# Kernel tuning notes

Hardware: AMD Instinct MI355X
Metric: run time of the kernel (lower is better)

## Reference

```python
import jax, jax.numpy as jnp
import numpy as np

B, N, D, O = 128, 256, 512, 512
EPS = 1e-5


def setup_inputs() -> dict:
    key = jax.random.key(0)
    ks = jax.random.split(key, 12)
    Observation = jax.random.normal(ks[0], (B, N, D), dtype=jnp.float32)
    mask = jax.random.bernoulli(ks[1], 0.7, (B, N))
    s = 0.02
    W1 = jax.random.normal(ks[2], (D, O), dtype=jnp.float32) * s
    W2 = jax.random.normal(ks[3], (O, O), dtype=jnp.float32) * s
    W3 = jax.random.normal(ks[4], (O, O), dtype=jnp.float32) * s
    g1 = 1.0 + 0.1 * jax.random.normal(ks[5], (D,), dtype=jnp.float32)
    b1 = 0.02 * jax.random.normal(ks[6], (D,), dtype=jnp.float32)
    g2 = 1.0 + 0.1 * jax.random.normal(ks[7], (O,), dtype=jnp.float32)
    b2 = 0.02 * jax.random.normal(ks[8], (O,), dtype=jnp.float32)
    g3 = 1.0 + 0.1 * jax.random.normal(ks[9], (O,), dtype=jnp.float32)
    b3 = 0.02 * jax.random.normal(ks[10], (O,), dtype=jnp.float32)
    return {"Observation": Observation, "mask": mask,
            "g1": g1, "b1": b1, "W1": W1,
            "g2": g2, "b2": b2, "W2": W2,
            "g3": g3, "b3": b3, "W3": W3}


def layer_norm(x, g, b):
    m = jnp.mean(x, axis=-1, keepdims=True)
    v = jnp.mean(jnp.square(x - m), axis=-1, keepdims=True)
    return (x - m) * jax.lax.rsqrt(v + EPS) * g + b


def reference(Observation, mask, g1, b1, W1, g2, b2, W2, g3, b3, W3):
    Bv, Nv, Dv = Observation.shape
    # _grant_at_least_one_valid: force element 0 valid if a row is all-invalid
    all_invalid = ~jnp.any(mask, axis=1)  # [B]
    mask = mask | (all_invalid[:, None] & (jnp.arange(Nv) == 0)[None, :])
    x = Observation.reshape(-1, Dv)  # [B*N, D]
    # Block 1: LN -> Linear (no bias) -> Tanh (dropout is eval identity)
    h1 = jnp.tanh(layer_norm(x, g1, b1) @ W1)
    # Block 2
    h2 = jnp.tanh(layer_norm(h1, g2, b2) @ W2)
    # Block 3 with residual input (h2 + h1), no activation
    o3 = layer_norm(h2 + h1, g3, b3) @ W3  # [B*N, O]
    fill = jnp.finfo(o3.dtype).min
    o3 = jnp.where(mask.reshape(-1, 1), o3, fill)
    out = jax.nn.softmax(o3.reshape(Bv, Nv, -1), axis=1)
    return jnp.nan_to_num(out, nan=0.0)
```

## Files before the change

kernel.cpp:

```cpp
#include <hip/hip_runtime.h>


#define NN 256

typedef _Float16 f16;
typedef __attribute__((ext_vector_type(4))) _Float16 f16x4;
typedef __attribute__((ext_vector_type(8))) _Float16 f16x8;
typedef __attribute__((ext_vector_type(4))) float f32x4;

#define XS    520
#define EPS32 516

__device__ __forceinline__ float fast_tanh(float x) {
  float e = __expf(2.f * x);
  return 1.f - 2.f * __builtin_amdgcn_rcpf(e + 1.f);
}
__device__ __forceinline__ void async_copy16(const void* g, void* l) {
  __builtin_amdgcn_global_load_lds(
      (const __attribute__((address_space(1))) unsigned int*)g,
      (__attribute__((address_space(3))) unsigned int*)l, 16, 0, 0);
}

__global__ void prep_w_kernel(const float* __restrict__ W1, const float* __restrict__ W2,
                              const float* __restrict__ W3, f16* __restrict__ WT) {
  int idx = blockIdx.x * 256 + threadIdx.x;
  int s   = idx >> 18;
  int rem = idx & 0x3FFFF;
  int o   = rem >> 9;
  int d   = rem & 511;
  const float* W = (s == 0) ? W1 : (s == 1) ? W2 : W3;
  WT[idx] = (f16)W[d * 512 + o];
}

__device__ __forceinline__ void stage_b(const f16* __restrict__ Bg, f16* __restrict__ dst,
                                        int wv, int lane, int c) {
  #pragma unroll
  for (int q = 0; q < 4; ++q) {
    int r0 = wv * 64 + q * 16;
    const f16* gb = Bg + (((size_t)(r0 + (lane >> 2))) << 9) + c * 32 + (lane & 3) * 8;
    async_copy16(gb, dst + r0 * 32);
  }
}

__global__ __launch_bounds__(512, 2) void mega_kernel(
    const float* __restrict__ Obs,
    const float* __restrict__ g1, const float* __restrict__ b1,
    const f16* __restrict__ WT,
    const float* __restrict__ g2, const float* __restrict__ b2,
    const float* __restrict__ g3, const float* __restrict__ b3,
    float* __restrict__ outF) {
  __shared__ __align__(16) char smem[136704];
  f16* sX  = (f16*)smem;
  f16* sB0 = (f16*)(smem + 66560);
  f16* sB1 = (f16*)(smem + 99328);
  float2* sPart = (float2*)(smem + 132096);
  float2* sStat = (float2*)(smem + 136192);

  int t = threadIdx.x, lane = t & 63, wv = t >> 6;
  int row16 = lane & 15, quad = lane >> 4;
  int rBase = blockIdx.x * 64;

  stage_b(WT, sB0, wv, lane, 0);

  {
    float4 w0 = *(const float4*)(g1 + lane * 4);
    float4 u0 = *(const float4*)(b1 + lane * 4);
    float4 w1 = *(const float4*)(g1 + 256 + lane * 4);
    float4 u1 = *(const float4*)(b1 + 256 + lane * 4);
    #pragma unroll
    for (int p = 0; p < 8; ++p) {
      int row = wv * 8 + p;
      const float* x = Obs + (((size_t)(rBase + row)) << 9);
      float4 v0 = *(const float4*)(x + lane * 4);
      float4 v1 = *(const float4*)(x + 256 + lane * 4);
      float s = v0.x + v0.y + v0.z + v0.w + v1.x + v1.y + v1.z + v1.w;
      float q = v0.x*v0.x + v0.y*v0.y + v0.z*v0.z + v0.w*v0.w
              + v1.x*v1.x + v1.y*v1.y + v1.z*v1.z + v1.w*v1.w;
      #pragma unroll
      for (int off = 1; off < 64; off <<= 1) {
        s += __shfl_xor(s, off, 64);
        q += __shfl_xor(q, off, 64);
      }
      float mean = s * (1.f / 512.f);
      float var  = q * (1.f / 512.f) - mean * mean;
      float inv  = 1.f / sqrtf(var + 1e-5f);
      f16x4 o0, o1;
      o0[0] = (f16)((v0.x - mean) * inv * w0.x + u0.x);
      o0[1] = (f16)((v0.y - mean) * inv * w0.y + u0.y);
      o0[2] = (f16)((v0.z - mean) * inv * w0.z + u0.z);
      o0[3] = (f16)((v0.w - mean) * inv * w0.w + u0.w);
      o1[0] = (f16)((v1.x - mean) * inv * w1.x + u1.x);
      o1[1] = (f16)((v1.y - mean) * inv * w1.y + u1.y);
      o1[2] = (f16)((v1.z - mean) * inv * w1.z + u1.z);
      o1[3] = (f16)((v1.w - mean) * inv * w1.w + u1.w);
      *(f16x4*)&sX[row * XS + lane * 4] = o0;
      *(f16x4*)&sX[row * XS + 256 + lane * 4] = o1;
    }
  }

  f32x4 acc[4][4];
  f16x4 h1s[4][4];

  __syncthreads();

  for (int g = 0; g < 3; ++g) {
    const f16* Bg = WT + ((size_t)g << 18);

    #pragma unroll
    for (int mi = 0; mi < 4; ++mi)
      #pragma unroll
      for (int ni = 0; ni < 4; ++ni)
        acc[mi][ni] = (f32x4){0.f, 0.f, 0.f, 0.f};

    for (int c = 0; c < 16; ++c) {
      if (c < 15) stage_b(Bg, (c & 1) ? sB0 : sB1, wv, lane, c + 1);

      const f16* bb = (c & 1) ? sB1 : sB0;
      f16x8 af[4], bf[4];
      #pragma unroll
      for (int i = 0; i < 4; ++i) {
        int ar = i * 16 + row16;
        af[i] = *(const f16x8*)&sX[ar * XS + c * 32 + quad * 8];
        int br = wv * 64 + i * 16 + row16;
        bf[i] = *(const f16x8*)&bb[br * 32 + quad * 8];
      }
      #pragma unroll
      for (int mi = 0; mi < 4; ++mi)
        #pragma unroll
        for (int ni = 0; ni < 4; ++ni)
          acc[mi][ni] = __builtin_amdgcn_mfma_f32_16x16x32_f16(af[mi], bf[ni], acc[mi][ni], 0, 0, 0);

      __syncthreads();
    }

    if (g == 2) {
      float* sE = (float*)smem;
      #pragma unroll
      for (int half = 0; half < 2; ++half) {
        #pragma unroll
        for (int mi = 0; mi < 2; ++mi) {
          int rt = half * 2 + mi;
          #pragma unroll
          for (int ni = 0; ni < 4; ++ni) {
            int col = wv * 64 + ni * 16 + row16;
            #pragma unroll
            for (int rg = 0; rg < 4; ++rg)
              sE[(mi * 16 + quad * 4 + rg) * EPS32 + col] = acc[rt][ni][rg];
          }
        }
        __syncthreads();
        #pragma unroll
        for (int i = 0; i < 8; ++i) {
          int gi = t + i * 512;
          int row = gi >> 7, cg = (gi & 127) * 4;
          f32x4 v = *(const f32x4*)&sE[row * EPS32 + cg];
          *(f32x4*)&outF[(((size_t)(rBase + half * 32 + row)) << 9) + cg] = v;
        }
        __syncthreads();
      }
    } else {
      #pragma unroll
      for (int mi = 0; mi < 4; ++mi)
        #pragma unroll
        for (int ni = 0; ni < 4; ++ni)
          #pragma unroll
          for (int rg = 0; rg < 4; ++rg)
            acc[mi][ni][rg] = fast_tanh(acc[mi][ni][rg]);

      if (g == 0) {
        #pragma unroll
        for (int mi = 0; mi < 4; ++mi)
          #pragma unroll
          for (int ni = 0; ni < 4; ++ni) {
            f16x4 h;
            #pragma unroll
            for (int rg = 0; rg < 4; ++rg) h[rg] = (f16)acc[mi][ni][rg];
            h1s[mi][ni] = h;
          }
      } else {
        #pragma unroll
        for (int mi = 0; mi < 4; ++mi)
          #pragma unroll
          for (int ni = 0; ni < 4; ++ni)
            #pragma unroll
            for (int rg = 0; rg < 4; ++rg)
              acc[mi][ni][rg] += (float)h1s[mi][ni][rg];
      }

      stage_b(WT + ((size_t)(g + 1) << 18), sB0, wv, lane, 0);

      const float* gp = (g == 0) ? g2 : g3;
      const float* bp = (g == 0) ? b2 : b3;
      float gva[4], bva[4];
      #pragma unroll
      for (int ni = 0; ni < 4; ++ni) {
        int col = wv * 64 + ni * 16 + row16;
        gva[ni] = gp[col]; bva[ni] = bp[col];
      }

      #pragma unroll
      for (int mi = 0; mi < 4; ++mi)
        #pragma unroll
        for (int rg = 0; rg < 4; ++rg) {
          float s = 0.f, q = 0.f;
          #pragma unroll
          for (int ni = 0; ni < 4; ++ni) {
            float v = acc[mi][ni][rg];
            s += v; q += v * v;
          }
          #pragma unroll
          for (int off = 1; off < 16; off <<= 1) {
            s += __shfl_xor(s, off, 16);
            q += __shfl_xor(q, off, 16);
          }
          if (row16 == 0)
            sPart[wv * 64 + mi * 16 + quad * 4 + rg] = make_float2(s, q);
        }
      __syncthreads();
      if (t < 64) {
        float s = 0.f, q = 0.f;
        #pragma unroll
        for (int w = 0; w < 8; ++w) {
          float2 p = sPart[w * 64 + t];
          s += p.x; q += p.y;
        }
        float mean = s * (1.f / 512.f);
        float var  = q * (1.f / 512.f) - mean * mean;
        sStat[t] = make_float2(mean, 1.f / sqrtf(var + 1e-5f));
      }
      __syncthreads();

      #pragma unroll
      for (int mi = 0; mi < 4; ++mi)
        #pragma unroll
        for (int rg = 0; rg < 4; ++rg) {
          int row = mi * 16 + quad * 4 + rg;
          float2 st = sStat[row];
          #pragma unroll
          for (int ni = 0; ni < 4; ++ni) {
            int col = wv * 64 + ni * 16 + row16;
            sX[row * XS + col] = (f16)((acc[mi][ni][rg] - st.x) * st.y * gva[ni] + bva[ni]);
          }
        }
      __syncthreads();
    }
  }
}

__global__ __launch_bounds__(256, 2) void softmax_kernel(const float* __restrict__ o3,
                                                         const int* __restrict__ mask,
                                                         float* __restrict__ out) {
  __shared__ float sz[NN * 64];
  __shared__ float sredm[4 * 64];
  __shared__ float sreds[4 * 64];
  __shared__ int   smask[NN];

  int b  = blockIdx.x >> 3;
  int oc = blockIdx.x & 7;
  int t  = threadIdx.x;
  int o_l = t & 63;
  int n_h = t >> 6;

  int mt = mask[b * NN + t];
  int any = __syncthreads_or(mt);
  smask[t] = (t == 0 && !any) ? 1 : mt;
  __syncthreads();

  const float* src = o3 + (((size_t)(b * NN)) << 9) + oc * 64;
  #pragma unroll 4
  for (int j = 0; j < 64; ++j) {
    int n = j * 4 + n_h;
    float v = src[((size_t)n << 9) + o_l];
    sz[n * 64 + o_l] = smask[n] ? v : -3.4e38f;
  }
  __syncthreads();

  float mx = -3.4e38f;
  #pragma unroll 8
  for (int i = 0; i < 64; ++i)
    mx = fmaxf(mx, sz[(n_h * 64 + i) * 64 + o_l]);
  sredm[n_h * 64 + o_l] = mx;
  __syncthreads();
  float m4 = fmaxf(fmaxf(sredm[o_l], sredm[64 + o_l]),
                   fmaxf(sredm[128 + o_l], sredm[192 + o_l]));

  float sm = 0.f;
  #pragma unroll 8
  for (int i = 0; i < 64; ++i)
    sm += __expf(sz[(n_h * 64 + i) * 64 + o_l] - m4);
  sreds[n_h * 64 + o_l] = sm;
  __syncthreads();
  float tot = sreds[o_l] + sreds[64 + o_l] + sreds[128 + o_l] + sreds[192 + o_l];
  float inv = 1.f / tot;

  float* dst = out + (((size_t)(b * NN)) << 9) + oc * 64;
  #pragma unroll 4
  for (int j = 0; j < 64; ++j) {
    int n = j * 4 + n_h;
    dst[((size_t)n << 9) + o_l] = __expf(sz[n * 64 + o_l] - m4) * inv;
  }
}

extern "C" void kernel_launch(void* const* d_in, const int* in_sizes, int n_in,
                              void* d_out, int out_size, void* d_ws, size_t ws_size,
                              hipStream_t stream) {
  const float* Obs = (const float*)d_in[0];
  const int*   msk = (const int*)d_in[1];
  const float* g1  = (const float*)d_in[2];
  const float* b1  = (const float*)d_in[3];
  const float* W1  = (const float*)d_in[4];
  const float* g2  = (const float*)d_in[5];
  const float* b2  = (const float*)d_in[6];
  const float* W2  = (const float*)d_in[7];
  const float* g3  = (const float*)d_in[8];
  const float* b3  = (const float*)d_in[9];
  const float* W3  = (const float*)d_in[10];
  float* out = (float*)d_out;

  char* ws = (char*)d_ws;
  const size_t MB = 1u << 20;
  float* Lg = (float*)ws;
  f16*   WT = (f16*)(ws + 64 * MB);

  prep_w_kernel<<<3072, 256, 0, stream>>>(W1, W2, W3, WT);
  mega_kernel<<<512, 512, 0, stream>>>(Obs, g1, b1, WT, g2, b2, g3, b3, Lg);
  softmax_kernel<<<1024, 256, 0, stream>>>(Lg, msk, out);
}
```

Before: 325.4 us.

## Load weight fragments directly into registers and keep softmax columns in registers

The GEMM loop no longer stages weight tiles through LDS with async copies. Each wave now loads its B fragments straight from global memory (L2) into registers, double-buffering them across k-steps. This removes the per-step barriers and shrinks LDS from about 137KB to 71KB, which may allow more blocks per CU, but makes the MFMA loop depend on global-load latency. The softmax kernel is also rewritten to hold each thread's 16 float4 values in registers with vectorized loads and stores, replacing the large LDS staging buffer.

```diff
diff --git a/kernel.cpp b/kernel.cpp
--- a/kernel.cpp
+++ b/kernel.cpp
@@ -14,11 +14,6 @@
 __device__ __forceinline__ float fast_tanh(float x) {
   float e = __expf(2.f * x);
   return 1.f - 2.f * __builtin_amdgcn_rcpf(e + 1.f);
-}
-__device__ __forceinline__ void async_copy16(const void* g, void* l) {
-  __builtin_amdgcn_global_load_lds(
-      (const __attribute__((address_space(1))) unsigned int*)g,
-      (__attribute__((address_space(3))) unsigned int*)l, 16, 0, 0);
 }
 
 __global__ void prep_w_kernel(const float* __restrict__ W1, const float* __restrict__ W2,
@@ -32,14 +27,17 @@
   WT[idx] = (f16)W[d * 512 + o];
 }
 
-__device__ __forceinline__ void stage_b(const f16* __restrict__ Bg, f16* __restrict__ dst,
-                                        int wv, int lane, int c) {
-  #pragma unroll
-  for (int q = 0; q < 4; ++q) {
-    int r0 = wv * 64 + q * 16;
-    const f16* gb = Bg + (((size_t)(r0 + (lane >> 2))) << 9) + c * 32 + (lane & 3) * 8;
-    async_copy16(gb, dst + r0 * 32);
-  }
+__device__ __forceinline__ void gemm_step(f32x4 acc[4][4], const f16* __restrict__ sXb,
+                                          const f16x8 bf[4], int c) {
+  f16x8 af[4];
+  #pragma unroll
+  for (int i = 0; i < 4; ++i)
+    af[i] = *(const f16x8*)&sXb[i * 16 * XS + c * 32];
+  #pragma unroll
+  for (int mi = 0; mi < 4; ++mi)
+    #pragma unroll
+    for (int ni = 0; ni < 4; ++ni)
+      acc[mi][ni] = __builtin_amdgcn_mfma_f32_16x16x32_f16(af[mi], bf[ni], acc[mi][ni], 0, 0, 0);
 }
 
 __global__ __launch_bounds__(512, 2) void mega_kernel(
@@ -49,18 +47,24 @@
     const float* __restrict__ g2, const float* __restrict__ b2,
     const float* __restrict__ g3, const float* __restrict__ b3,
     float* __restrict__ outF) {
-  __shared__ __align__(16) char smem[136704];
-  f16* sX  = (f16*)smem;
-  f16* sB0 = (f16*)(smem + 66560);
-  f16* sB1 = (f16*)(smem + 99328);
-  float2* sPart = (float2*)(smem + 132096);
-  float2* sStat = (float2*)(smem + 136192);
+  __shared__ __align__(16) char smem[71168];
+  f16* sX = (f16*)smem;
+  float2* sPart = (float2*)(smem + 66560);
+  float2* sStat = (float2*)(smem + 70656);
 
   int t = threadIdx.x, lane = t & 63, wv = t >> 6;
   int row16 = lane & 15, quad = lane >> 4;
   int rBase = blockIdx.x * 64;
 
-  stage_b(WT, sB0, wv, lane, 0);
+  const f16* sXb = sX + row16 * XS + quad * 8;
+  const f16* bw  = WT + (((size_t)(wv * 64 + row16)) << 9) + quad * 8;
+
+  f32x4 acc[4][4];
+  f16x8 bfA[4], bfB[4];
+  f16x4 h1s[4][4];
+
+  #pragma unroll
+  for (int i = 0; i < 4; ++i) bfA[i] = *(const f16x8*)(bw + i * 8192);
 
   {
     float4 w0 = *(const float4*)(g1 + lane * 4);
@@ -97,43 +101,31 @@
       *(f16x4*)&sX[row * XS + 256 + lane * 4] = o1;
     }
   }
-
-  f32x4 acc[4][4];
-  f16x4 h1s[4][4];
-
   __syncthreads();
 
   for (int g = 0; g < 3; ++g) {
-    const f16* Bg = WT + ((size_t)g << 18);
-
     #pragma unroll
     for (int mi = 0; mi < 4; ++mi)
       #pragma unroll
       for (int ni = 0; ni < 4; ++ni)
         acc[mi][ni] = (f32x4){0.f, 0.f, 0.f, 0.f};
 
-    for (int c = 0; c < 16; ++c) {
-      if (c < 15) stage_b(Bg, (c & 1) ? sB0 : sB1, wv, lane, c + 1);
-
-      const f16* bb = (c & 1) ? sB1 : sB0;
-      f16x8 af[4], bf[4];
-      #pragma unroll
-      for (int i = 0; i < 4; ++i) {
-        int ar = i * 16 + row16;
-        af[i] = *(const f16x8*)&sX[ar * XS + c * 32 + quad * 8];
-        int br = wv * 64 + i * 16 + row16;
-        bf[i] = *(const f16x8*)&bb[br * 32 + quad * 8];
-      }
-      #pragma unroll
-      for (int mi = 0; mi < 4; ++mi)
-        #pragma unroll
-        for (int ni = 0; ni < 4; ++ni)
-          acc[mi][ni] = __builtin_amdgcn_mfma_f32_16x16x32_f16(af[mi], bf[ni], acc[mi][ni], 0, 0, 0);
-
+    #pragma unroll
+    for (int c = 0; c < 16; c += 2) {
+      #pragma unroll
+      for (int i = 0; i < 4; ++i)
+        bfB[i] = *(const f16x8*)(bw + i * 8192 + (c + 1) * 32);
+      gemm_step(acc, sXb, bfA, c);
+      if (c + 2 < 16) {
+        #pragma unroll
+        for (int i = 0; i < 4; ++i)
+          bfA[i] = *(const f16x8*)(bw + i * 8192 + (c + 2) * 32);
+      }
+      gemm_step(acc, sXb, bfB, c + 1);
+    }
+
+    if (g == 2) {
       __syncthreads();
-    }
-
-    if (g == 2) {
       float* sE = (float*)smem;
       #pragma unroll
       for (int half = 0; half < 2; ++half) {
@@ -187,8 +179,6 @@
               acc[mi][ni][rg] += (float)h1s[mi][ni][rg];
       }
 
-      stage_b(WT + ((size_t)(g + 1) << 18), sB0, wv, lane, 0);
-
       const float* gp = (g == 0) ? g2 : g3;
       const float* bp = (g == 0) ? b2 : b3;
       float gva[4], bva[4];
@@ -228,6 +218,11 @@
         float var  = q * (1.f / 512.f) - mean * mean;
         sStat[t] = make_float2(mean, 1.f / sqrtf(var + 1e-5f));
       }
+
+      bw += 262144;
+      #pragma unroll
+      for (int i = 0; i < 4; ++i) bfA[i] = *(const f16x8*)(bw + i * 8192);
+
       __syncthreads();
 
       #pragma unroll
@@ -250,54 +245,73 @@
 __global__ __launch_bounds__(256, 2) void softmax_kernel(const float* __restrict__ o3,
                                                          const int* __restrict__ mask,
                                                          float* __restrict__ out) {
-  __shared__ float sz[NN * 64];
-  __shared__ float sredm[4 * 64];
-  __shared__ float sreds[4 * 64];
-  __shared__ int   smask[NN];
+  __shared__ float4 smx[16][16];
+  __shared__ float4 sms[16][16];
+  __shared__ int    smask[NN];
 
   int b  = blockIdx.x >> 3;
   int oc = blockIdx.x & 7;
   int t  = threadIdx.x;
-  int o_l = t & 63;
-  int n_h = t >> 6;
+  int c4 = t & 15;
+  int nh = t >> 4;
+
+  const float4* src = (const float4*)(o3 + (((size_t)(b * NN)) << 9)) + oc * 16 + c4;
+  float4 v[16];
+  #pragma unroll
+  for (int j = 0; j < 16; ++j)
+    v[j] = src[(size_t)(nh + 16 * j) * 128];
 
   int mt = mask[b * NN + t];
   int any = __syncthreads_or(mt);
   smask[t] = (t == 0 && !any) ? 1 : mt;
   __syncthreads();
 
-  const float* src = o3 + (((size_t)(b * NN)) << 9) + oc * 64;
-  #pragma unroll 4
-  for (int j = 0; j < 64; ++j) {
-    int n = j * 4 + n_h;
-    float v = src[((size_t)n << 9) + o_l];
-    sz[n * 64 + o_l] = smask[n] ? v : -3.4e38f;
-  }
+  const float NEG = -3.4e38f;
+  #pragma unroll
+  for (int j = 0; j < 16; ++j)
+    if (!smask[nh + 16 * j]) v[j] = (float4){NEG, NEG, NEG, NEG};
+
+  float4 m4 = v[0];
+  #pragma unroll
+  for (int j = 1; j < 16; ++j) {
+    m4.x = fmaxf(m4.x, v[j].x); m4.y = fmaxf(m4.y, v[j].y);
+    m4.z = fmaxf(m4.z, v[j].z); m4.w = fmaxf(m4.w, v[j].w);
+  }
+  smx[nh][c4] = m4;
   __syncthreads();
-
-  float mx = -3.4e38f;
-  #pragma unroll 8
-  for (int i = 0; i < 64; ++i)
-    mx = fmaxf(mx, sz[(n_h * 64 + i) * 64 + o_l]);
-  sredm[n_h * 64 + o_l] = mx;
+  float4 mm = smx[0][c4];
+  #pragma unroll
+  for (int k = 1; k < 16; ++k) {
+    float4 o = smx[k][c4];
+    mm.x = fmaxf(mm.x, o.x); mm.y = fmaxf(mm.y, o.y);
+    mm.z = fmaxf(mm.z, o.z); mm.w = fmaxf(mm.w, o.w);
+  }
+
+  float4 s4 = {0.f, 0.f, 0.f, 0.f};
+  #pragma unroll
+  for (int j = 0; j < 16; ++j) {
+    s4.x += __expf(v[j].x - mm.x); s4.y += __expf(v[j].y - mm.y);
+    s4.z += __expf(v[j].z - mm.z); s4.w += __expf(v[j].w - mm.w);
+  }
+  sms[nh][c4] = s4;
   __syncthreads();
-  float m4 = fmaxf(fmaxf(sredm[o_l], sredm[64 + o_l]),
-                   fmaxf(sredm[128 + o_l], sredm[192 + o_l]));
-
-  float sm = 0.f;
-  #pragma unroll 8
-  for (int i = 0; i < 64; ++i)
-    sm += __expf(sz[(n_h * 64 + i) * 64 + o_l] - m4);
-  sreds[n_h * 64 + o_l] = sm;
-  __syncthreads();
-  float tot = sreds[o_l] + sreds[64 + o_l] + sreds[128 + o_l] + sreds[192 + o_l];
-  float inv = 1.f / tot;
-
-  float* dst = out + (((size_t)(b * NN)) << 9) + oc * 64;
-  #pragma unroll 4
-  for (int j = 0; j < 64; ++j) {
-    int n = j * 4 + n_h;
-    dst[((size_t)n << 9) + o_l] = __expf(sz[n * 64 + o_l] - m4) * inv;
+  float4 tot = sms[0][c4];
+  #pragma unroll
+  for (int k = 1; k < 16; ++k) {
+    float4 o = sms[k][c4];
+    tot.x += o.x; tot.y += o.y; tot.z += o.z; tot.w += o.w;
+  }
+  float4 inv = {1.f / tot.x, 1.f / tot.y, 1.f / tot.z, 1.f / tot.w};
+
+  float4* dst = (float4*)(out + (((size_t)(b * NN)) << 9)) + oc * 16 + c4;
+  #pragma unroll
+  for (int j = 0; j < 16; ++j) {
+    float4 r;
+    r.x = __expf(v[j].x - mm.x) * inv.x;
+    r.y = __expf(v[j].y - mm.y) * inv.y;
+    r.z = __expf(v[j].z - mm.z) * inv.z;
+    r.w = __expf(v[j].w - mm.w) * inv.w;
+    dst[(size_t)(nh + 16 * j) * 128] = r;
   }
 }
 
```

After: 317.2 us. 1.03x faster.
